# Performance work log

Hardware: AMD Instinct MI355X
Metric: run time of the kernel (lower is better)

Reference implementation:

```python
import jax, jax.numpy as jnp
import numpy as np

B, S, D = 8, 1024, 1152
H, HD = 16, 72  # num_heads, head_dim

def setup_inputs() -> dict:
    key = jax.random.key(0)
    ks = jax.random.split(key, 7)
    hidden_states = jax.random.normal(ks[0], (B, S, D), dtype=jnp.float32)
    cos = jax.random.uniform(ks[1], (S, HD), dtype=jnp.float32)
    sin = jax.random.uniform(ks[2], (S, HD), dtype=jnp.float32)
    qkv_w = jax.random.normal(ks[3], (3 * D, D), dtype=jnp.float32) * 0.02
    qkv_b = jnp.zeros((3 * D,), dtype=jnp.float32)
    proj_w = jax.random.normal(ks[4], (D, D), dtype=jnp.float32) * 0.02
    proj_b = jnp.zeros((D,), dtype=jnp.float32)
    return {"hidden_states": hidden_states, "cos": cos, "sin": sin,
            "qkv_w": qkv_w, "qkv_b": qkv_b, "proj_w": proj_w, "proj_b": proj_b}

def _rotate_half(x):
    x1, x2 = jnp.split(x, 2, axis=-1)
    return jnp.concatenate((-x2, x1), axis=-1)

def reference(hidden_states, cos, sin, qkv_w, qkv_b, proj_w, proj_b):
    b, s, d = hidden_states.shape
    # fused QKV projection
    qkv = hidden_states @ qkv_w.T + qkv_b            # [B,S,3D]
    qkv = qkv.reshape(b, s, 3, H, HD)
    qkv = jnp.transpose(qkv, (2, 0, 3, 1, 4))        # [3,B,H,S,HD]
    q, k, v = qkv[0], qkv[1], qkv[2]
    # rotary embedding, cos/sin broadcast [1,1,S,HD]
    c = cos[None, None, :, :]
    sn = sin[None, None, :, :]
    q = q * c + _rotate_half(q) * sn
    k = k * c + _rotate_half(k) * sn
    # SDPA
    scale = HD ** -0.5
    scores = jnp.einsum('bhqd,bhkd->bhqk', q, k) * scale
    probs = jax.nn.softmax(scores, axis=-1)
    attn = jnp.einsum('bhqk,bhkd->bhqd', probs, v)   # [B,H,S,HD]
    attn = jnp.transpose(attn, (0, 2, 1, 3)).reshape(b, s, d)
    return attn @ proj_w.T + proj_b
```

## Files before the change

### kernel.cpp

```cpp
#include <hip/hip_runtime.h>
#include <hip/hip_bf16.h>


typedef __attribute__((ext_vector_type(8))) short short8;
typedef __attribute__((ext_vector_type(4))) float f32x4;

__device__ __forceinline__ unsigned int f2bf(float f) {
    unsigned int u = __float_as_uint(f);
    return (u + 0x7FFFu + ((u >> 16) & 1u)) >> 16;
}
__device__ __forceinline__ float bf2f(unsigned short u) {
    return __uint_as_float((unsigned int)u << 16);
}

__device__ __forceinline__ unsigned int pk_bf16(float a, float b) {
    unsigned int r;
    asm("v_cvt_pk_bf16_f32 %0, %1, %2" : "=v"(r) : "v"(a), "v"(b));
    return r;
}

__device__ __forceinline__ void stout(float* C, size_t idx, float v) { C[idx] = v; }
__device__ __forceinline__ void stout(__hip_bfloat16* C, size_t idx, float v) {
    C[idx] = __float2bfloat16(v);
}

__device__ __forceinline__ void async_cp16(const void* g, void* l) {
    __builtin_amdgcn_global_load_lds((const __attribute__((address_space(1))) void*)g,
                                     (__attribute__((address_space(3))) void*)l, 16, 0, 0);
}

__global__ void f32_to_bf16_pair(
    const float* __restrict__ s0, unsigned short* __restrict__ d0, int n0_4,
    const float* __restrict__ s1, unsigned short* __restrict__ d1, int n1_4,
    unsigned short* __restrict__ dz, int nz_4)
{
    int i = blockIdx.x * 256 + threadIdx.x;
    if (i < n0_4) {
        float4 f = ((const float4*)s0)[i];
        ushort4 r;
        r.x = (unsigned short)f2bf(f.x);
        r.y = (unsigned short)f2bf(f.y);
        r.z = (unsigned short)f2bf(f.z);
        r.w = (unsigned short)f2bf(f.w);
        ((ushort4*)d0)[i] = r;
        return;
    }
    i -= n0_4;
    if (i < n1_4) {
        float4 f = ((const float4*)s1)[i];
        ushort4 r;
        r.x = (unsigned short)f2bf(f.x);
        r.y = (unsigned short)f2bf(f.y);
        r.z = (unsigned short)f2bf(f.z);
        r.w = (unsigned short)f2bf(f.w);
        ((ushort4*)d1)[i] = r;
        return;
    }
    i -= n1_4;
    if (i < nz_4) {
        ushort4 z; z.x = 0; z.y = 0; z.z = 0; z.w = 0;
        ((ushort4*)dz)[i] = z;
    }
}

template <int ISB, int H>
__device__ __forceinline__ void stage_ht(const unsigned short* __restrict__ g, int ldg,
                                         int k0, unsigned short* l, int w, int lane)
{
#pragma unroll
    for (int t = 0; t < 2; t++) {
        const int c  = w * 2 + t;
        const int r0 = ISB ? ((c >> 2) * 64 + H * 32 + (c & 3) * 8)
                           : ((c & 8) * 16 + H * 64 + (c & 7) * 8);
        const int rl = r0 + (lane >> 3);
        const int gg = (lane & 7) ^ (lane >> 3);
        async_cp16(g + (size_t)rl * ldg + k0 + gg * 8, l + r0 * 64);
    }
}

#define LDA(MH, SRC)                                                              \
    _Pragma("unroll") for (int mi = 0; mi < 4; ++mi) {                            \
        Af[mi][0] = *(const short8*)((SRC) + aRow + (MH) * 4096 + mi * 1024 + g0); \
        Af[mi][1] = *(const short8*)((SRC) + aRow + (MH) * 4096 + mi * 1024 + g1); \
    }

#define LDB(DST, NH, SRC)                                                         \
    _Pragma("unroll") for (int ni = 0; ni < 2; ++ni) {                            \
        DST[ni][0] = *(const short8*)((SRC) + bRow + (NH) * 2048 + ni * 1024 + g0); \
        DST[ni][1] = *(const short8*)((SRC) + bRow + (NH) * 2048 + ni * 1024 + g1); \
    }

#define MFMAS(MH, NH, PB)                                                         \
    __builtin_amdgcn_s_setprio(1);                                                \
    _Pragma("unroll") for (int mi = 0; mi < 4; ++mi)                              \
    _Pragma("unroll") for (int ni = 0; ni < 2; ++ni) {                            \
        acc[(MH) * 4 + mi][(NH) * 2 + ni] = __builtin_amdgcn_mfma_f32_16x16x32_bf16( \
            Af[mi][0], PB[ni][0], acc[(MH) * 4 + mi][(NH) * 2 + ni], 0, 0, 0);    \
        acc[(MH) * 4 + mi][(NH) * 2 + ni] = __builtin_amdgcn_mfma_f32_16x16x32_bf16( \
            Af[mi][1], PB[ni][1], acc[(MH) * 4 + mi][(NH) * 2 + ni], 0, 0, 0);    \
    }                                                                             \
    __builtin_amdgcn_s_setprio(0);

#define MIDBAR()                                                   \
    do {                                                           \
        __builtin_amdgcn_s_barrier();                              \
        asm volatile("s_waitcnt lgkmcnt(0)" ::: "memory");         \
        __builtin_amdgcn_sched_barrier(0);                         \
    } while (0)

#define ENDBAR()                                                   \
    do {                                                           \
        __builtin_amdgcn_s_barrier();                              \
        __builtin_amdgcn_sched_barrier(0);                         \
    } while (0)

template <typename OT>
__global__ __launch_bounds__(512, 2) void gemm_bt_256(
    const __hip_bfloat16* __restrict__ Abf,
    const __hip_bfloat16* __restrict__ Bbf,
    const float* __restrict__ bias,
    OT* __restrict__ C,
    int M, int Nreal, int K)
{
    __shared__ __align__(16) unsigned short smem[2][2][256 * 64];

    const int tid  = threadIdx.x;
    const int lane = tid & 63;
    const int w    = tid >> 6;
    const int wm   = w >> 2;
    const int wn   = w & 3;
    const int q    = lane >> 4;
    const int fr   = lane & 15;
    const int xr   = fr & 7;

    const int nwg = gridDim.x * gridDim.y;
    const int lin = blockIdx.y * gridDim.x + blockIdx.x;
    const int swz = (lin & 7) * (nwg >> 3) + (lin >> 3);
    const int bn  = (swz % gridDim.x) * 256;
    const int bm  = (swz / gridDim.x) * 256;

    const unsigned short* Ag = (const unsigned short*)Abf + (size_t)bm * K;
    const unsigned short* Bg = (const unsigned short*)Bbf + (size_t)bn * K;

    unsigned short* s00 = &smem[0][0][0];
    unsigned short* s01 = &smem[0][1][0];
    unsigned short* s10 = &smem[1][0][0];
    unsigned short* s11 = &smem[1][1][0];

    const int NT = K >> 6;
    const int NI = NT >> 1;

    const int aRow = (wm * 128 + fr) * 64;
    const int bRow = (wn * 64 + fr) * 64;
    const int g0   = ((0 * 4 + q) ^ xr) * 8;
    const int g1   = ((1 * 4 + q) ^ xr) * 8;

    f32x4 acc[8][4];
#pragma unroll
    for (int i = 0; i < 8; i++)
#pragma unroll
        for (int j = 0; j < 4; j++) acc[i][j] = (f32x4){0.f, 0.f, 0.f, 0.f};

    short8 Af[4][2], Bf0[2][2], Bf1[2][2];

    stage_ht<0, 0>(Ag, K, 0, s00, w, lane);
    stage_ht<0, 1>(Ag, K, 0, s00, w, lane);
    stage_ht<1, 0>(Bg, K, 0, s01, w, lane);
    stage_ht<1, 1>(Bg, K, 0, s01, w, lane);
    stage_ht<0, 0>(Ag, K, 64, s10, w, lane);
    stage_ht<1, 1>(Bg, K, 64, s10 + 16384, w, lane);
    stage_ht<0, 1>(Ag, K, 64, s10, w, lane);
    asm volatile("s_waitcnt vmcnt(6)" ::: "memory");
    ENDBAR();

#pragma unroll 1
    for (int i = 0; i < NI; i++) {
        const int k1 = (2 * i + 1) * 64;
        const int t2 = 2 * i + 2, t3 = 2 * i + 3;
        const int k2 = (t2 < NT ? t2 : NT - 1) * 64;
        const int k3 = (t3 < NT ? t3 : NT - 1) * 64;

        LDA(0, s00);
        LDB(Bf0, 0, s01);
        stage_ht<1, 0>(Bg, K, k1, s11, w, lane);
        asm volatile("s_waitcnt lgkmcnt(8)" ::: "memory");
        MIDBAR();
        MFMAS(0, 0, Bf0);
        ENDBAR();

        LDB(Bf1, 1, s01);
        stage_ht<0, 0>(Ag, K, k2, s00, w, lane);
        MIDBAR();
        MFMAS(0, 1, Bf1);
        ENDBAR();

        LDA(1, s00);
        stage_ht<1, 1>(Bg, K, k2, s01, w, lane);
        MIDBAR();
        MFMAS(1, 1, Bf1);
        ENDBAR();

        stage_ht<0, 1>(Ag, K, k2, s00, w, lane);
        asm volatile("s_waitcnt vmcnt(6)" ::: "memory");
        MIDBAR();
        MFMAS(1, 0, Bf0);
        ENDBAR();

        LDA(0, s10);
        LDB(Bf0, 0, s11);
        stage_ht<1, 0>(Bg, K, k2, s01, w, lane);
        asm volatile("s_waitcnt lgkmcnt(8)" ::: "memory");
        MIDBAR();
        MFMAS(0, 0, Bf0);
        ENDBAR();

        LDB(Bf1, 1, s11);
        stage_ht<0, 0>(Ag, K, k3, s10, w, lane);
        MIDBAR();
        MFMAS(0, 1, Bf1);
        ENDBAR();

        LDA(1, s10);
        stage_ht<1, 1>(Bg, K, k3, s11, w, lane);
        MIDBAR();
        MFMAS(1, 1, Bf1);
        ENDBAR();

        stage_ht<0, 1>(Ag, K, k3, s10, w, lane);
        asm volatile("s_waitcnt vmcnt(6)" ::: "memory");
        MIDBAR();
        MFMAS(1, 0, Bf0);
        ENDBAR();
    }

#pragma unroll
    for (int mf = 0; mf < 8; mf++) {
        const int row = bm + wm * 128 + mf * 16 + q * 4;
#pragma unroll
        for (int nf = 0; nf < 4; nf++) {
            const int col = bn + wn * 64 + nf * 16 + fr;
            if (col < Nreal) {
                const float bv = bias[col];
#pragma unroll
                for (int r = 0; r < 4; r++)
                    stout(C, (size_t)(row + r) * Nreal + col, acc[mf][nf][r] + bv);
            }
        }
    }
}

__global__ void rope_v_prep(
    const __hip_bfloat16* __restrict__ qkv,
    const float* __restrict__ cosp,
    const float* __restrict__ sinp,
    __hip_bfloat16* __restrict__ Qo,
    __hip_bfloat16* __restrict__ Ko,
    __hip_bfloat16* __restrict__ Vt)
{
    __shared__ __align__(16) unsigned short T[64 * 72];
    const int tid = threadIdx.x;
    const int bh = blockIdx.x >> 4;
    const int st = blockIdx.x & 15;
    const int b = bh >> 4, h = bh & 15;
    const size_t row0 = ((size_t)b * 1024 + st * 64) * 3456;

    const unsigned short* vsrc = (const unsigned short*)qkv + row0 + 2304 + h * 72;
#pragma unroll
    for (int k = 0; k < 3; k++) {
        const int c = tid + k * 256;
        if (c < 576) {
            const int s = c / 9, off = (c % 9) * 8;
            *(uint4*)&T[c * 8] = *(const uint4*)(vsrc + (size_t)s * 3456 + off);
        }
    }

    const unsigned short* qkvp = (const unsigned short*)qkv;
    const float QS = 0.17002324f;
#pragma unroll
    for (int k = 0; k < 3; k++) {
        const int idx = tid + k * 256;
        if (idx < 576) {
            const int sl = idx / 9, iq = idx % 9;
            const int i0 = iq * 4;
            const int sg = st * 64 + sl;
            const unsigned short* qrow = qkvp + row0 + (size_t)sl * 3456 + h * 72 + i0;

            ushort4 ql = *(const ushort4*)(qrow);
            ushort4 qh = *(const ushort4*)(qrow + 36);
            ushort4 kl = *(const ushort4*)(qrow + 1152);
            ushort4 kh = *(const ushort4*)(qrow + 1188);
            float4 cl = *(const float4*)(cosp + sg * 72 + i0);
            float4 ch = *(const float4*)(cosp + sg * 72 + i0 + 36);
            float4 nl = *(const float4*)(sinp + sg * 72 + i0);
            float4 nh = *(const float4*)(sinp + sg * 72 + i0 + 36);

            unsigned short qlv[4] = {ql.x, ql.y, ql.z, ql.w};
            unsigned short qhv[4] = {qh.x, qh.y, qh.z, qh.w};
            unsigned short klv[4] = {kl.x, kl.y, kl.z, kl.w};
            unsigned short khv[4] = {kh.x, kh.y, kh.z, kh.w};
            float clv[4] = {cl.x, cl.y, cl.z, cl.w};
            float chv[4] = {ch.x, ch.y, ch.z, ch.w};
            float nlv[4] = {nl.x, nl.y, nl.z, nl.w};
            float nhv[4] = {nh.x, nh.y, nh.z, nh.w};

            unsigned short qol[4], qoh[4], kol[4], koh[4];
#pragma unroll
            for (int j = 0; j < 4; j++) {
                const float qa = bf2f(qlv[j]), qb = bf2f(qhv[j]);
                const float ka = bf2f(klv[j]), kb = bf2f(khv[j]);
                qol[j] = (unsigned short)f2bf((qa * clv[j] - qb * nlv[j]) * QS);
                qoh[j] = (unsigned short)f2bf((qb * chv[j] + qa * nhv[j]) * QS);
                kol[j] = (unsigned short)f2bf(ka * clv[j] - kb * nlv[j]);
                koh[j] = (unsigned short)f2bf(kb * chv[j] + ka * nhv[j]);
            }
            unsigned short* qob = (unsigned short*)Qo + ((size_t)bh * 1024 + sg) * 72 + i0;
            unsigned short* kob = (unsigned short*)Ko + ((size_t)bh * 1024 + sg) * 72 + i0;
            *(ushort4*)qob        = (ushort4){qol[0], qol[1], qol[2], qol[3]};
            *(ushort4*)(qob + 36) = (ushort4){qoh[0], qoh[1], qoh[2], qoh[3]};
            *(ushort4*)kob        = (ushort4){kol[0], kol[1], kol[2], kol[3]};
            *(ushort4*)(kob + 36) = (ushort4){koh[0], koh[1], koh[2], koh[3]};
        }
    }

    __syncthreads();

    unsigned short* dst = (unsigned short*)Vt + (size_t)(bh * 16 + st) * 72 * 64;
#pragma unroll
    for (int k = 0; k < 9; k++) {
        const int o = tid + k * 256;
        const int d = o >> 5;
        const int sl = (o & 31) * 2;
        ushort2 v;
        v.x = T[sl * 72 + d];
        v.y = T[(sl + 1) * 72 + d];
        const int col = ((((sl >> 3) ^ (d & 7)) << 3)) + (sl & 7);
        *(ushort2*)&dst[d * 64 + col] = v;
    }
}

__device__ __forceinline__ void attn_stage(const unsigned short* kt, const unsigned short* vt,
                                           unsigned short* kl, unsigned short* vl,
                                           int w, int lane)
{
#pragma unroll
    for (int c = 0; c < 5; c++) {
        const int call = w + c * 4;
        if (call < 18) {
            const bool isv = (call >= 9);
            const int o = (isv ? call - 9 : call) * 512;
            const unsigned short* s = (isv ? vt : kt) + o + lane * 8;
            unsigned short* d = (isv ? vl : kl) + o;
            async_cp16(s, d);
        }
    }
}

__global__ __launch_bounds__(256, 2) void attn_mfma(
    const __hip_bfloat16* __restrict__ Q,
    const __hip_bfloat16* __restrict__ K,
    const __hip_bfloat16* __restrict__ Vt,
    __hip_bfloat16* __restrict__ O)
{
    __shared__ __align__(16) unsigned short KsA[2][64 * 72];
    __shared__ __align__(16) unsigned short VsA[2][72 * 64];
    __shared__ __align__(16) unsigned short Vones[8 * 64];
    __shared__ __align__(16) unsigned short Ps[4][32][72];

    const int tid  = threadIdx.x;
    const int lane = tid & 63;
    const int w    = tid >> 6;
    const int quad = lane >> 4;
    const int fr   = lane & 15;
    const int bh   = blockIdx.x & 127;
    const int qt   = blockIdx.x >> 7;
    const int qbase = qt * 128 + w * 32;

    const short8 z8 = (short8){0,0,0,0,0,0,0,0};

    for (int idx = tid; idx < 512; idx += 256)
        Vones[idx] = (idx < 64) ? (unsigned short)0x3F80 : (unsigned short)0;

    const unsigned short* qp = (const unsigned short*)Q + ((size_t)bh * 1024 + qbase + fr) * 72;
    short8 qf[2][3];
#pragma unroll
    for (int sub = 0; sub < 2; sub++) {
        const unsigned short* qs = qp + sub * 16 * 72;
        qf[sub][0] = *(const short8*)(qs + quad * 8);
        qf[sub][1] = *(const short8*)(qs + 32 + quad * 8);
        qf[sub][2] = (quad == 0) ? *(const short8*)(qs + 64) : z8;
    }

    f32x4 Oa[2][5];
#pragma unroll
    for (int sub = 0; sub < 2; sub++)
#pragma unroll
        for (int n = 0; n < 5; n++) Oa[sub][n] = (f32x4){0.f, 0.f, 0.f, 0.f};

    const unsigned short* kg0 = (const unsigned short*)K + (size_t)bh * 1024 * 72;
    const unsigned short* vg0 = (const unsigned short*)Vt + (size_t)bh * 16 * 72 * 64;

    attn_stage(kg0,        vg0,        &KsA[0][0], &VsA[0][0], w, lane);
    attn_stage(kg0 + 4608, vg0 + 4608, &KsA[1][0], &VsA[1][0], w, lane);
    __builtin_amdgcn_sched_barrier(0);

#pragma unroll 1
    for (int t = 0; t < 16; t++) {
        if (t < 15) {
            if (w < 2) asm volatile("s_waitcnt vmcnt(5)" ::: "memory");
            else       asm volatile("s_waitcnt vmcnt(4)" ::: "memory");
        } else {
            asm volatile("s_waitcnt vmcnt(0)" ::: "memory");
        }
        __builtin_amdgcn_sched_barrier(0);
        __builtin_amdgcn_s_barrier();

        const unsigned short* kb = (t & 1) ? &KsA[1][0] : &KsA[0][0];
        const unsigned short* vb = (t & 1) ? &VsA[1][0] : &VsA[0][0];

#pragma unroll
        for (int nt = 0; nt < 4; nt++) {
            const unsigned short* kr = kb + (nt * 16 + fr) * 72;
            short8 b0 = *(const short8*)(kr + quad * 8);
            short8 b1 = *(const short8*)(kr + 32 + quad * 8);
            short8 b2 = (quad == 0) ? *(const short8*)(kr + 64) : z8;
            f32x4 s0 = (f32x4){0.f, 0.f, 0.f, 0.f};
            f32x4 s1 = (f32x4){0.f, 0.f, 0.f, 0.f};
            __builtin_amdgcn_s_setprio(1);
            s0 = __builtin_amdgcn_mfma_f32_16x16x32_bf16(b0, qf[0][0], s0, 0, 0, 0);
            s1 = __builtin_amdgcn_mfma_f32_16x16x32_bf16(b0, qf[1][0], s1, 0, 0, 0);
            s0 = __builtin_amdgcn_mfma_f32_16x16x32_bf16(b1, qf[0][1], s0, 0, 0, 0);
            s1 = __builtin_amdgcn_mfma_f32_16x16x32_bf16(b1, qf[1][1], s1, 0, 0, 0);
            s0 = __builtin_amdgcn_mfma_f32_16x16x32_bf16(b2, qf[0][2], s0, 0, 0, 0);
            s1 = __builtin_amdgcn_mfma_f32_16x16x32_bf16(b2, qf[1][2], s1, 0, 0, 0);
            __builtin_amdgcn_s_setprio(0);
            uint2 p0, p1;
            p0.x = pk_bf16(__builtin_amdgcn_exp2f(s0[0]), __builtin_amdgcn_exp2f(s0[1]));
            p0.y = pk_bf16(__builtin_amdgcn_exp2f(s0[2]), __builtin_amdgcn_exp2f(s0[3]));
            p1.x = pk_bf16(__builtin_amdgcn_exp2f(s1[0]), __builtin_amdgcn_exp2f(s1[1]));
            p1.y = pk_bf16(__builtin_amdgcn_exp2f(s1[2]), __builtin_amdgcn_exp2f(s1[3]));
            *(uint2*)&Ps[w][fr][nt * 16 + quad * 4]      = p0;
            *(uint2*)&Ps[w][16 + fr][nt * 16 + quad * 4] = p1;
        }

#pragma unroll
        for (int ks = 0; ks < 2; ks++) {
            short8 ap0 = *(const short8*)&Ps[w][fr][ks * 32 + quad * 8];
            short8 ap1 = *(const short8*)&Ps[w][16 + fr][ks * 32 + quad * 8];
            const int jx8 = ((ks * 4 + quad) ^ (fr & 7)) * 8;
#pragma unroll
            for (int n = 0; n < 5; n++) {
                const unsigned short* p =
                    (n < 4) ? (vb + (n * 16 + fr) * 64 + jx8)
                            : ((fr < 8) ? (vb + (64 + fr) * 64 + jx8)
                                        : (&Vones[0] + (fr - 8) * 64 + jx8));
                short8 bv = *(const short8*)p;
                __builtin_amdgcn_s_setprio(1);
                Oa[0][n] = __builtin_amdgcn_mfma_f32_16x16x32_bf16(ap0, bv, Oa[0][n], 0, 0, 0);
                Oa[1][n] = __builtin_amdgcn_mfma_f32_16x16x32_bf16(ap1, bv, Oa[1][n], 0, 0, 0);
                __builtin_amdgcn_s_setprio(0);
            }
        }

        __builtin_amdgcn_s_barrier();
        __builtin_amdgcn_sched_barrier(0);

        if (t < 14) {
            unsigned short* kd = (t & 1) ? &KsA[1][0] : &KsA[0][0];
            unsigned short* vd = (t & 1) ? &VsA[1][0] : &VsA[0][0];
            attn_stage(kg0 + (size_t)(t + 2) * 4608, vg0 + (size_t)(t + 2) * 4608,
                       kd, vd, w, lane);
            __builtin_amdgcn_sched_barrier(0);
        }
    }

    const int lsrc = (lane & 48) | 8;
    const int b = bh >> 4, h = bh & 15;
    unsigned short* ob = (unsigned short*)O;
#pragma unroll
    for (int sub = 0; sub < 2; sub++) {
        float inv[4];
#pragma unroll
        for (int r = 0; r < 4; r++)
            inv[r] = 1.f / __shfl(Oa[sub][4][r], lsrc, 64);
#pragma unroll
        for (int n = 0; n < 5; n++) {
            const int d = n * 16 + fr;
            if (d < 72) {
#pragma unroll
                for (int r = 0; r < 4; r++) {
                    const size_t idx =
                        ((size_t)b * 1024 + qbase + sub * 16 + quad * 4 + r) * 1152 + h * 72 + d;
                    ob[idx] = (unsigned short)f2bf(Oa[sub][n][r] * inv[r]);
                }
            }
        }
    }
}

extern "C" void kernel_launch(void* const* d_in, const int* in_sizes, int n_in,
                              void* d_out, int out_size, void* d_ws, size_t ws_size,
                              hipStream_t stream)
{
    const float* hs     = (const float*)d_in[0];
    const float* cosp   = (const float*)d_in[1];
    const float* sinp   = (const float*)d_in[2];
    const float* qkv_w  = (const float*)d_in[3];
    const float* qkv_b  = (const float*)d_in[4];
    const float* proj_w = (const float*)d_in[5];
    const float* proj_b = (const float*)d_in[6];
    float* out = (float*)d_out;

    char* ws = (char*)d_ws;
    __hip_bfloat16* qkv_buf = (__hip_bfloat16*)ws;
    __hip_bfloat16* Qb = (__hip_bfloat16*)(ws + 56623104);
    __hip_bfloat16* Kb = Qb + 9437184;
    __hip_bfloat16* Vt = Kb + 9437184;
    __hip_bfloat16* Ab = qkv_buf;

    unsigned short* hs_bf = (unsigned short*)Qb;
    unsigned short* qw_bf = (unsigned short*)Kb;
    unsigned short* pw_bf = (unsigned short*)Qb;

    f32_to_bf16_pair<<<13248, 256, 0, stream>>>(hs, hs_bf, 2359296,
                                                qkv_w, qw_bf, 995328,
                                                qw_bf + 3981312, 36864);
    gemm_bt_256<__hip_bfloat16>
        <<<dim3(14, 32), 512, 0, stream>>>((const __hip_bfloat16*)hs_bf,
                                           (const __hip_bfloat16*)qw_bf,
                                           qkv_b, qkv_buf, 8192, 3456, 1152);
    rope_v_prep<<<2048, 256, 0, stream>>>(qkv_buf, cosp, sinp, Qb, Kb, Vt);
    attn_mfma<<<1024, 256, 0, stream>>>(Qb, Kb, Vt, Ab);
    f32_to_bf16_pair<<<1440, 256, 0, stream>>>(proj_w, pw_bf, 331776,
                                               nullptr, nullptr, 0,
                                               pw_bf + 1327104, 36864);
    gemm_bt_256<float>
        <<<dim3(5, 32), 512, 0, stream>>>((const __hip_bfloat16*)Ab,
                                          (const __hip_bfloat16*)pw_bf,
                                          proj_b, out, 8192, 1152, 1152);
}
```

Measured before the change: 302.6 us.

## Use 128-row tiles for output GEMM and single-buffer K in attention

Templates the GEMM on the M tile size and launches the output projection with 128x256 tiles. That doubles its grid from 160 to 320 workgroups, so more CUs are busy on the small N=1152 GEMM. The attention kernel drops K double-buffering: K is loaded into a single buffer after QK^T is done, and only V stays double-buffered. The freed LDS lets launch bounds rise to 3 blocks per CU. The costs are an extra barrier per iteration in attention, less prefetch distance for K, and lower arithmetic intensity per GEMM tile.

```diff
diff --git a/kernel.cpp b/kernel.cpp
--- a/kernel.cpp
+++ b/kernel.cpp
@@ -63,25 +63,46 @@
     }
 }
 
-template <int ISB, int H>
-__device__ __forceinline__ void stage_ht(const unsigned short* __restrict__ g, int ldg,
-                                         int k0, unsigned short* l, int w, int lane)
-{
-#pragma unroll
-    for (int t = 0; t < 2; t++) {
-        const int c  = w * 2 + t;
-        const int r0 = ISB ? ((c >> 2) * 64 + H * 32 + (c & 3) * 8)
-                           : ((c & 8) * 16 + H * 64 + (c & 7) * 8);
+template <int BM, int H>
+__device__ __forceinline__ void stage_a(const unsigned short* __restrict__ g, int ldg,
+                                        int k0, unsigned short* l, int w, int lane)
+{
+    if constexpr (BM == 256) {
+#pragma unroll
+        for (int t = 0; t < 2; t++) {
+            const int c  = w * 2 + t;
+            const int r0 = (c & 8) * 16 + H * 64 + (c & 7) * 8;
+            const int rl = r0 + (lane >> 3);
+            const int gg = (lane & 7) ^ (lane >> 3);
+            async_cp16(g + (size_t)rl * ldg + k0 + gg * 8, l + r0 * 64);
+        }
+    } else {
+        const int c  = w;
+        const int r0 = (c & 4) * 16 + H * 32 + (c & 3) * 8;
         const int rl = r0 + (lane >> 3);
         const int gg = (lane & 7) ^ (lane >> 3);
         async_cp16(g + (size_t)rl * ldg + k0 + gg * 8, l + r0 * 64);
     }
 }
 
-#define LDA(MH, SRC)                                                              \
-    _Pragma("unroll") for (int mi = 0; mi < 4; ++mi) {                            \
-        Af[mi][0] = *(const short8*)((SRC) + aRow + (MH) * 4096 + mi * 1024 + g0); \
-        Af[mi][1] = *(const short8*)((SRC) + aRow + (MH) * 4096 + mi * 1024 + g1); \
+template <int H>
+__device__ __forceinline__ void stage_b(const unsigned short* __restrict__ g, int ldg,
+                                        int k0, unsigned short* l, int w, int lane)
+{
+#pragma unroll
+    for (int t = 0; t < 2; t++) {
+        const int c  = w * 2 + t;
+        const int r0 = (c >> 2) * 64 + H * 32 + (c & 3) * 8;
+        const int rl = r0 + (lane >> 3);
+        const int gg = (lane & 7) ^ (lane >> 3);
+        async_cp16(g + (size_t)rl * ldg + k0 + gg * 8, l + r0 * 64);
+    }
+}
+
+#define LDA(MH, SRC)                                                                   \
+    _Pragma("unroll") for (int mi = 0; mi < MFRAG_; ++mi) {                            \
+        Af[mi][0] = *(const short8*)((SRC) + aRow + (MH) * (BM * 16) + mi * 1024 + g0); \
+        Af[mi][1] = *(const short8*)((SRC) + aRow + (MH) * (BM * 16) + mi * 1024 + g1); \
     }
 
 #define LDB(DST, NH, SRC)                                                         \
@@ -90,15 +111,15 @@
         DST[ni][1] = *(const short8*)((SRC) + bRow + (NH) * 2048 + ni * 1024 + g1); \
     }
 
-#define MFMAS(MH, NH, PB)                                                         \
-    __builtin_amdgcn_s_setprio(1);                                                \
-    _Pragma("unroll") for (int mi = 0; mi < 4; ++mi)                              \
-    _Pragma("unroll") for (int ni = 0; ni < 2; ++ni) {                            \
-        acc[(MH) * 4 + mi][(NH) * 2 + ni] = __builtin_amdgcn_mfma_f32_16x16x32_bf16( \
-            Af[mi][0], PB[ni][0], acc[(MH) * 4 + mi][(NH) * 2 + ni], 0, 0, 0);    \
-        acc[(MH) * 4 + mi][(NH) * 2 + ni] = __builtin_amdgcn_mfma_f32_16x16x32_bf16( \
-            Af[mi][1], PB[ni][1], acc[(MH) * 4 + mi][(NH) * 2 + ni], 0, 0, 0);    \
-    }                                                                             \
+#define MFMAS(MH, NH, PB)                                                              \
+    __builtin_amdgcn_s_setprio(1);                                                     \
+    _Pragma("unroll") for (int mi = 0; mi < MFRAG_; ++mi)                              \
+    _Pragma("unroll") for (int ni = 0; ni < 2; ++ni) {                                 \
+        acc[(MH) * MFRAG_ + mi][(NH) * 2 + ni] = __builtin_amdgcn_mfma_f32_16x16x32_bf16( \
+            Af[mi][0], PB[ni][0], acc[(MH) * MFRAG_ + mi][(NH) * 2 + ni], 0, 0, 0);    \
+        acc[(MH) * MFRAG_ + mi][(NH) * 2 + ni] = __builtin_amdgcn_mfma_f32_16x16x32_bf16( \
+            Af[mi][1], PB[ni][1], acc[(MH) * MFRAG_ + mi][(NH) * 2 + ni], 0, 0, 0);    \
+    }                                                                                  \
     __builtin_amdgcn_s_setprio(0);
 
 #define MIDBAR()                                                   \
@@ -114,7 +135,15 @@
         __builtin_amdgcn_sched_barrier(0);                         \
     } while (0)
 
-template <typename OT>
+#define GVMCNT()                                                          \
+    do {                                                                  \
+        if constexpr (BM == 256)                                          \
+            asm volatile("s_waitcnt vmcnt(6)" ::: "memory");              \
+        else                                                              \
+            asm volatile("s_waitcnt vmcnt(4)" ::: "memory");              \
+    } while (0)
+
+template <typename OT, int BM>
 __global__ __launch_bounds__(512, 2) void gemm_bt_256(
     const __hip_bfloat16* __restrict__ Abf,
     const __hip_bfloat16* __restrict__ Bbf,
@@ -122,7 +151,8 @@
     OT* __restrict__ C,
     int M, int Nreal, int K)
 {
-    __shared__ __align__(16) unsigned short smem[2][2][256 * 64];
+    constexpr int MFRAG_ = BM / 64;
+    __shared__ __align__(16) unsigned short smem[2][(BM + 256) * 64];
 
     const int tid  = threadIdx.x;
     const int lane = tid & 63;
@@ -137,40 +167,40 @@
     const int lin = blockIdx.y * gridDim.x + blockIdx.x;
     const int swz = (lin & 7) * (nwg >> 3) + (lin >> 3);
     const int bn  = (swz % gridDim.x) * 256;
-    const int bm  = (swz / gridDim.x) * 256;
+    const int bm  = (swz / gridDim.x) * BM;
 
     const unsigned short* Ag = (const unsigned short*)Abf + (size_t)bm * K;
     const unsigned short* Bg = (const unsigned short*)Bbf + (size_t)bn * K;
 
-    unsigned short* s00 = &smem[0][0][0];
-    unsigned short* s01 = &smem[0][1][0];
-    unsigned short* s10 = &smem[1][0][0];
-    unsigned short* s11 = &smem[1][1][0];
+    unsigned short* s00 = &smem[0][0];
+    unsigned short* s01 = &smem[0][BM * 64];
+    unsigned short* s10 = &smem[1][0];
+    unsigned short* s11 = &smem[1][BM * 64];
 
     const int NT = K >> 6;
     const int NI = NT >> 1;
 
-    const int aRow = (wm * 128 + fr) * 64;
+    const int aRow = (wm * (BM / 2) + fr) * 64;
     const int bRow = (wn * 64 + fr) * 64;
     const int g0   = ((0 * 4 + q) ^ xr) * 8;
     const int g1   = ((1 * 4 + q) ^ xr) * 8;
 
-    f32x4 acc[8][4];
-#pragma unroll
-    for (int i = 0; i < 8; i++)
+    f32x4 acc[2 * MFRAG_][4];
+#pragma unroll
+    for (int i = 0; i < 2 * MFRAG_; i++)
 #pragma unroll
         for (int j = 0; j < 4; j++) acc[i][j] = (f32x4){0.f, 0.f, 0.f, 0.f};
 
-    short8 Af[4][2], Bf0[2][2], Bf1[2][2];
-
-    stage_ht<0, 0>(Ag, K, 0, s00, w, lane);
-    stage_ht<0, 1>(Ag, K, 0, s00, w, lane);
-    stage_ht<1, 0>(Bg, K, 0, s01, w, lane);
-    stage_ht<1, 1>(Bg, K, 0, s01, w, lane);
-    stage_ht<0, 0>(Ag, K, 64, s10, w, lane);
-    stage_ht<1, 1>(Bg, K, 64, s10 + 16384, w, lane);
-    stage_ht<0, 1>(Ag, K, 64, s10, w, lane);
-    asm volatile("s_waitcnt vmcnt(6)" ::: "memory");
+    short8 Af[MFRAG_][2], Bf0[2][2], Bf1[2][2];
+
+    stage_a<BM, 0>(Ag, K, 0, s00, w, lane);
+    stage_a<BM, 1>(Ag, K, 0, s00, w, lane);
+    stage_b<0>(Bg, K, 0, s01, w, lane);
+    stage_b<1>(Bg, K, 0, s01, w, lane);
+    stage_a<BM, 0>(Ag, K, 64, s10, w, lane);
+    stage_b<1>(Bg, K, 64, s11, w, lane);
+    stage_a<BM, 1>(Ag, K, 64, s10, w, lane);
+    GVMCNT();
     ENDBAR();
 
 #pragma unroll 1
@@ -182,60 +212,60 @@
 
         LDA(0, s00);
         LDB(Bf0, 0, s01);
-        stage_ht<1, 0>(Bg, K, k1, s11, w, lane);
+        stage_b<0>(Bg, K, k1, s11, w, lane);
         asm volatile("s_waitcnt lgkmcnt(8)" ::: "memory");
         MIDBAR();
         MFMAS(0, 0, Bf0);
         ENDBAR();
 
         LDB(Bf1, 1, s01);
-        stage_ht<0, 0>(Ag, K, k2, s00, w, lane);
+        stage_a<BM, 0>(Ag, K, k2, s00, w, lane);
         MIDBAR();
         MFMAS(0, 1, Bf1);
         ENDBAR();
 
         LDA(1, s00);
-        stage_ht<1, 1>(Bg, K, k2, s01, w, lane);
+        stage_b<1>(Bg, K, k2, s01, w, lane);
         MIDBAR();
         MFMAS(1, 1, Bf1);
         ENDBAR();
 
-        stage_ht<0, 1>(Ag, K, k2, s00, w, lane);
-        asm volatile("s_waitcnt vmcnt(6)" ::: "memory");
+        stage_a<BM, 1>(Ag, K, k2, s00, w, lane);
+        GVMCNT();
         MIDBAR();
         MFMAS(1, 0, Bf0);
         ENDBAR();
 
         LDA(0, s10);
         LDB(Bf0, 0, s11);
-        stage_ht<1, 0>(Bg, K, k2, s01, w, lane);
+        stage_b<0>(Bg, K, k2, s01, w, lane);
         asm volatile("s_waitcnt lgkmcnt(8)" ::: "memory");
         MIDBAR();
         MFMAS(0, 0, Bf0);
         ENDBAR();
 
         LDB(Bf1, 1, s11);
-        stage_ht<0, 0>(Ag, K, k3, s10, w, lane);
+        stage_a<BM, 0>(Ag, K, k3, s10, w, lane);
         MIDBAR();
         MFMAS(0, 1, Bf1);
         ENDBAR();
 
         LDA(1, s10);
-        stage_ht<1, 1>(Bg, K, k3, s11, w, lane);
+        stage_b<1>(Bg, K, k3, s11, w, lane);
         MIDBAR();
         MFMAS(1, 1, Bf1);
         ENDBAR();
 
-        stage_ht<0, 1>(Ag, K, k3, s10, w, lane);
-        asm volatile("s_waitcnt vmcnt(6)" ::: "memory");
+        stage_a<BM, 1>(Ag, K, k3, s10, w, lane);
+        GVMCNT();
         MIDBAR();
         MFMAS(1, 0, Bf0);
         ENDBAR();
     }
 
 #pragma unroll
-    for (int mf = 0; mf < 8; mf++) {
-        const int row = bm + wm * 128 + mf * 16 + q * 4;
+    for (int mf = 0; mf < 2 * MFRAG_; mf++) {
+        const int row = bm + wm * (BM / 2) + mf * 16 + q * 4;
 #pragma unroll
         for (int nf = 0; nf < 4; nf++) {
             const int col = bn + wn * 64 + nf * 16 + fr;
@@ -338,30 +368,23 @@
     }
 }
 
-__device__ __forceinline__ void attn_stage(const unsigned short* kt, const unsigned short* vt,
-                                           unsigned short* kl, unsigned short* vl,
-                                           int w, int lane)
-{
-#pragma unroll
-    for (int c = 0; c < 5; c++) {
-        const int call = w + c * 4;
-        if (call < 18) {
-            const bool isv = (call >= 9);
-            const int o = (isv ? call - 9 : call) * 512;
-            const unsigned short* s = (isv ? vt : kt) + o + lane * 8;
-            unsigned short* d = (isv ? vl : kl) + o;
-            async_cp16(s, d);
-        }
-    }
-}
-
-__global__ __launch_bounds__(256, 2) void attn_mfma(
+__device__ __forceinline__ void dma9(const unsigned short* g, unsigned short* l,
+                                     int w, int lane)
+{
+#pragma unroll
+    for (int c = 0; c < 3; c++) {
+        const int i = w + c * 4;
+        if (i < 9) async_cp16(g + i * 512 + lane * 8, l + i * 512);
+    }
+}
+
+__global__ __launch_bounds__(256, 3) void attn_mfma(
     const __hip_bfloat16* __restrict__ Q,
     const __hip_bfloat16* __restrict__ K,
     const __hip_bfloat16* __restrict__ Vt,
     __hip_bfloat16* __restrict__ O)
 {
-    __shared__ __align__(16) unsigned short KsA[2][64 * 72];
+    __shared__ __align__(16) unsigned short Ks[64 * 72];
     __shared__ __align__(16) unsigned short VsA[2][72 * 64];
     __shared__ __align__(16) unsigned short Vones[8 * 64];
     __shared__ __align__(16) unsigned short Ps[4][32][72];
@@ -399,27 +422,27 @@
     const unsigned short* kg0 = (const unsigned short*)K + (size_t)bh * 1024 * 72;
     const unsigned short* vg0 = (const unsigned short*)Vt + (size_t)bh * 16 * 72 * 64;
 
-    attn_stage(kg0,        vg0,        &KsA[0][0], &VsA[0][0], w, lane);
-    attn_stage(kg0 + 4608, vg0 + 4608, &KsA[1][0], &VsA[1][0], w, lane);
+    dma9(kg0, Ks, w, lane);
+    dma9(vg0, &VsA[0][0], w, lane);
+    dma9(vg0 + 4608, &VsA[1][0], w, lane);
     __builtin_amdgcn_sched_barrier(0);
 
 #pragma unroll 1
     for (int t = 0; t < 16; t++) {
         if (t < 15) {
-            if (w < 2) asm volatile("s_waitcnt vmcnt(5)" ::: "memory");
-            else       asm volatile("s_waitcnt vmcnt(4)" ::: "memory");
+            if (w == 0) asm volatile("s_waitcnt vmcnt(3)" ::: "memory");
+            else        asm volatile("s_waitcnt vmcnt(2)" ::: "memory");
         } else {
             asm volatile("s_waitcnt vmcnt(0)" ::: "memory");
         }
         __builtin_amdgcn_sched_barrier(0);
         __builtin_amdgcn_s_barrier();
 
-        const unsigned short* kb = (t & 1) ? &KsA[1][0] : &KsA[0][0];
-        const unsigned short* vb = (t & 1) ? &VsA[1][0] : &VsA[0][0];
+        const unsigned short* vb = &VsA[t & 1][0];
 
 #pragma unroll
         for (int nt = 0; nt < 4; nt++) {
-            const unsigned short* kr = kb + (nt * 16 + fr) * 72;
+            const unsigned short* kr = Ks + (nt * 16 + fr) * 72;
             short8 b0 = *(const short8*)(kr + quad * 8);
             short8 b1 = *(const short8*)(kr + 32 + quad * 8);
             short8 b2 = (quad == 0) ? *(const short8*)(kr + 64) : z8;
@@ -442,6 +465,13 @@
             *(uint2*)&Ps[w][16 + fr][nt * 16 + quad * 4] = p1;
         }
 
+        __builtin_amdgcn_s_barrier();
+        __builtin_amdgcn_sched_barrier(0);
+        if (t < 15) {
+            dma9(kg0 + (size_t)(t + 1) * 4608, Ks, w, lane);
+            __builtin_amdgcn_sched_barrier(0);
+        }
+
 #pragma unroll
         for (int ks = 0; ks < 2; ks++) {
             short8 ap0 = *(const short8*)&Ps[w][fr][ks * 32 + quad * 8];
@@ -463,12 +493,8 @@
 
         __builtin_amdgcn_s_barrier();
         __builtin_amdgcn_sched_barrier(0);
-
         if (t < 14) {
-            unsigned short* kd = (t & 1) ? &KsA[1][0] : &KsA[0][0];
-            unsigned short* vd = (t & 1) ? &VsA[1][0] : &VsA[0][0];
-            attn_stage(kg0 + (size_t)(t + 2) * 4608, vg0 + (size_t)(t + 2) * 4608,
-                       kd, vd, w, lane);
+            dma9(vg0 + (size_t)(t + 2) * 4608, &VsA[t & 1][0], w, lane);
             __builtin_amdgcn_sched_barrier(0);
         }
     }
@@ -524,7 +550,7 @@
     f32_to_bf16_pair<<<13248, 256, 0, stream>>>(hs, hs_bf, 2359296,
                                                 qkv_w, qw_bf, 995328,
                                                 qw_bf + 3981312, 36864);
-    gemm_bt_256<__hip_bfloat16>
+    gemm_bt_256<__hip_bfloat16, 256>
         <<<dim3(14, 32), 512, 0, stream>>>((const __hip_bfloat16*)hs_bf,
                                            (const __hip_bfloat16*)qw_bf,
                                            qkv_b, qkv_buf, 8192, 3456, 1152);
@@ -533,8 +559,8 @@
     f32_to_bf16_pair<<<1440, 256, 0, stream>>>(proj_w, pw_bf, 331776,
                                                nullptr, nullptr, 0,
                                                pw_bf + 1327104, 36864);
-    gemm_bt_256<float>
-        <<<dim3(5, 32), 512, 0, stream>>>((const __hip_bfloat16*)Ab,
+    gemm_bt_256<float, 128>
+        <<<dim3(5, 64), 512, 0, stream>>>((const __hip_bfloat16*)Ab,
                                           (const __hip_bfloat16*)pw_bf,
                                           proj_b, out, 8192, 1152, 1152);
 }
```

Result: no change. 303.3 us (+0.2%).
